# Optimization experiments

Hardware: AMD Instinct MI355X
Metric: run time of the kernel (lower is better)

The kernel has to match this reference:

```python
import jax, jax.numpy as jnp
import numpy as np

N = 50000
E = 800000
IN_CH = 128
HID = 32
HEADS = 4
OUT_CH = 40
LEAKY = 0.2
BN_EPS = 1e-5


def _gat_layer(x, src, dst, W, a_src, a_dst, b, n_nodes, concat):
    # x: [N, F_in], W: [F_in, H*C], a_src/a_dst: [H, C], b: [H*C] or [C]
    H, C = a_src.shape
    h = (x @ W).reshape(n_nodes, H, C)                      # [N, H, C]
    e_s = jnp.einsum('nhc,hc->nh', h, a_src)                # [N, H]
    e_d = jnp.einsum('nhc,hc->nh', h, a_dst)                # [N, H]
    e = e_s[src] + e_d[dst]                                 # [E, H]
    e = jnp.where(e > 0, e, LEAKY * e)                      # LeakyReLU
    # segment softmax over incoming edges of each destination node
    m = jax.ops.segment_max(e, dst, num_segments=n_nodes)   # [N, H]
    ex = jnp.exp(e - m[dst])
    s = jax.ops.segment_sum(ex, dst, num_segments=n_nodes)  # [N, H]
    alpha = ex / s[dst]                                     # [E, H]
    out = jax.ops.segment_sum(h[src] * alpha[:, :, None], dst,
                              num_segments=n_nodes)         # [N, H, C]
    out = out.reshape(n_nodes, H * C) if concat else out.mean(axis=1)
    return out + b


def setup_inputs() -> dict:
    key = jax.random.key(0)
    ks = jax.random.split(key, 16)
    d1 = HEADS * HID  # 128
    inp = {
        'x': jax.random.normal(ks[0], (N, IN_CH), dtype=jnp.float32),
        'edge_index': jax.random.randint(ks[1], (2, E), 0, N, dtype=jnp.int64),
        # conv1 params (heads=4, concat)
        'W1': jax.random.normal(ks[2], (IN_CH, d1), dtype=jnp.float32) * 0.1,
        'a1_src': jax.random.normal(ks[3], (HEADS, HID), dtype=jnp.float32) * 0.1,
        'a1_dst': jax.random.normal(ks[4], (HEADS, HID), dtype=jnp.float32) * 0.1,
        'b1': jnp.zeros((d1,), dtype=jnp.float32),
        # BatchNorm1d(128) in eval mode
        'bn_gamma': jnp.ones((d1,), dtype=jnp.float32),
        'bn_beta': jnp.zeros((d1,), dtype=jnp.float32),
        'bn_mean': jax.random.normal(ks[5], (d1,), dtype=jnp.float32) * 0.1,
        'bn_var': jax.random.uniform(ks[6], (d1,), minval=0.5, maxval=1.5, dtype=jnp.float32),
        # conv2 params (heads=1, concat=False)
        'W2': jax.random.normal(ks[7], (d1, OUT_CH), dtype=jnp.float32) * 0.1,
        'a2_src': jax.random.normal(ks[8], (1, OUT_CH), dtype=jnp.float32) * 0.1,
        'a2_dst': jax.random.normal(ks[9], (1, OUT_CH), dtype=jnp.float32) * 0.1,
        'b2': jnp.zeros((OUT_CH,), dtype=jnp.float32),
    }
    return inp


def reference(x, edge_index, W1, a1_src, a1_dst, b1, bn_gamma, bn_beta,
              bn_mean, bn_var, W2, a2_src, a2_dst, b2):
    n = x.shape[0]
    loops = jnp.arange(n, dtype=edge_index.dtype)
    src = jnp.concatenate([edge_index[0], loops])  # PyG GATConv adds self-loops
    dst = jnp.concatenate([edge_index[1], loops])
    h = _gat_layer(x, src, dst, W1, a1_src, a1_dst, b1, n, concat=True)
    h = (h - bn_mean) / jnp.sqrt(bn_var + BN_EPS) * bn_gamma + bn_beta  # BN eval
    h = jax.nn.elu(h)
    # dropout is identity in eval mode
    out = _gat_layer(h, src, dst, W2, a2_src, a2_dst, b2, n, concat=False)
    return jax.nn.log_softmax(out, axis=1)
```

## Files before the change

### kernel.cpp

```cpp
#include <hip/hip_runtime.h>
#include <hip/hip_bf16.h>
#include <math.h>

#define NN 50000
#define NE 800000
#define ETOT (NE + NN)
#define LEAKY 0.2f
#define BN_EPS 1e-5f

#define NB 256
#define BSZ 196
#define NBB 128
#define EPB ((ETOT + NBB - 1) / NBB)

#define BN1 144
#define BN2 48

typedef unsigned short u16;
typedef unsigned int u32;
typedef short s16;
typedef __attribute__((ext_vector_type(8))) short bf16x8;
typedef __attribute__((ext_vector_type(4))) float f32x4;

__device__ __forceinline__ float bf2f(u32 u) {
    union { u32 i; float f; } x; x.i = u << 16; return x.f;
}
__device__ __forceinline__ float bf2f_lo(u32 u) {
    union { u32 i; float f; } x; x.i = u << 16; return x.f;
}
__device__ __forceinline__ float bf2f_hi(u32 u) {
    union { u32 i; float f; } x; x.i = u & 0xffff0000u; return x.f;
}
__device__ __forceinline__ u16 f2bf(float f) {
    __hip_bfloat16 b = __float2bfloat16(f);
    return *reinterpret_cast<u16*>(&b);
}


__global__ __launch_bounds__(256) void k_binA(const int* __restrict__ ei,
                                              int* __restrict__ cnt) {
    __shared__ int hist[NB];
    int t = threadIdx.x;
    for (int i = t; i < NB; i += 256) hist[i] = 0;
    __syncthreads();
    int e0 = blockIdx.x * EPB, e1 = min(e0 + EPB, ETOT);
    for (int e = e0 + t; e < e1; e += 256) {
        int dst = (e < NE) ? ei[NE + e] : (e - NE);
        atomicAdd(&hist[dst / BSZ], 1);
    }
    __syncthreads();
    for (int b = t; b < NB; b += 256) cnt[b * NBB + blockIdx.x] = hist[b];
}

__global__ __launch_bounds__(256) void k_scanA(const int* __restrict__ in,
                                               int* __restrict__ out,
                                               int* __restrict__ bsums, int n) {
    __shared__ int sh[256];
    int t = threadIdx.x;
    int i = blockIdx.x * 256 + t;
    int v = (i < n) ? in[i] : 0;
    sh[t] = v;
    __syncthreads();
    #pragma unroll
    for (int off = 1; off < 256; off <<= 1) {
        int u = (t >= off) ? sh[t - off] : 0;
        __syncthreads();
        sh[t] += u;
        __syncthreads();
    }
    if (i < n) out[i] = sh[t] - v;
    if (t == 255) bsums[blockIdx.x] = sh[t];
}

__global__ __launch_bounds__(256) void k_scanB(int* __restrict__ bsums, int nb) {
    __shared__ int sh[256];
    int t = threadIdx.x;
    int v = (t < nb) ? bsums[t] : 0;
    sh[t] = v;
    __syncthreads();
    #pragma unroll
    for (int off = 1; off < 256; off <<= 1) {
        int u = (t >= off) ? sh[t - off] : 0;
        __syncthreads();
        sh[t] += u;
        __syncthreads();
    }
    if (t < nb) bsums[t] = sh[t] - v;
}

__global__ void k_scanC(int* __restrict__ out, const int* __restrict__ bsums, int n) {
    int i = blockIdx.x * blockDim.x + threadIdx.x;
    if (i < n) out[i] += bsums[i >> 8];
}

__global__ __launch_bounds__(256) void k_binB(const int* __restrict__ ei,
                                              const int* __restrict__ excl,
                                              u32* __restrict__ packed) {
    __shared__ int cur[NB];
    int t = threadIdx.x;
    for (int b = t; b < NB; b += 256) cur[b] = excl[b * NBB + blockIdx.x];
    __syncthreads();
    int e0 = blockIdx.x * EPB, e1 = min(e0 + EPB, ETOT);
    for (int e = e0 + t; e < e1; e += 256) {
        int src, dst;
        if (e < NE) { src = ei[e]; dst = ei[NE + e]; }
        else        { src = e - NE; dst = e - NE; }
        int pos = atomicAdd(&cur[dst / BSZ], 1);
        packed[pos] = ((u32)src << 16) | (u32)dst;
    }
}

__global__ __launch_bounds__(256) void k_binC(const u32* __restrict__ packed,
                                              const int* __restrict__ excl,
                                              int* __restrict__ offsets,
                                              int* __restrict__ ssrc) {
    __shared__ int hist[256];
    __shared__ int sc[256];
    __shared__ int cur[256];
    int b = blockIdx.x, t = threadIdx.x;
    int n0 = b * BSZ;
    int base = excl[b * NBB];
    int next = (b < NB - 1) ? excl[(b + 1) * NBB] : ETOT;
    int total = next - base;
    hist[t] = 0;
    __syncthreads();
    for (int i = t; i < total; i += 256) {
        int dst = (int)(packed[base + i] & 0xffffu);
        atomicAdd(&hist[dst - n0], 1);
    }
    __syncthreads();
    int v = hist[t];
    sc[t] = v;
    __syncthreads();
    #pragma unroll
    for (int off = 1; off < 256; off <<= 1) {
        int u = (t >= off) ? sc[t - off] : 0;
        __syncthreads();
        sc[t] += u;
        __syncthreads();
    }
    int exl = sc[t] - v;
    int node = n0 + t;
    if (t <= BSZ && node <= NN) {
        if (t < BSZ || node == NN) offsets[node] = base + exl;
    }
    cur[t] = exl;
    __syncthreads();
    for (int i = t; i < total; i += 256) {
        u32 pv = packed[base + i];
        int dst = (int)(pv & 0xffffu);
        int pos = atomicAdd(&cur[dst - n0], 1);
        ssrc[base + pos] = (int)(pv >> 16);
    }
}

__global__ void k_prep(const float* __restrict__ W1, const float* __restrict__ a1s,
                       const float* __restrict__ a1d, const float* __restrict__ W2,
                       const float* __restrict__ a2s, const float* __restrict__ a2d,
                       u16* __restrict__ Wt1, u16* __restrict__ Wt2) {
    int tid = blockIdx.x * blockDim.x + threadIdx.x;
    int nth = gridDim.x * blockDim.x;
    for (int idx = tid; idx < BN1 * 128; idx += nth) {
        int n = idx >> 7, k = idx & 127;
        float v = 0.f;
        if (n < 128) v = W1[k * 128 + n];
        else if (n < 132) {
            int h = n - 128; float s = 0.f;
            for (int c = 0; c < 32; ++c) s += W1[k * 128 + h * 32 + c] * a1s[h * 32 + c];
            v = s;
        } else if (n < 136) {
            int h = n - 132; float s = 0.f;
            for (int c = 0; c < 32; ++c) s += W1[k * 128 + h * 32 + c] * a1d[h * 32 + c];
            v = s;
        }
        Wt1[idx] = f2bf(v);
    }
    for (int idx = tid; idx < BN2 * 128; idx += nth) {
        int n = idx >> 7, k = idx & 127;
        float v = 0.f;
        if (n < 40) v = W2[k * 40 + n];
        else if (n == 40) { float s = 0.f; for (int c = 0; c < 40; ++c) s += W2[k * 40 + c] * a2s[c]; v = s; }
        else if (n == 41) { float s = 0.f; for (int c = 0; c < 40; ++c) s += W2[k * 40 + c] * a2d[c]; v = s; }
        Wt2[idx] = f2bf(v);
    }
}

__global__ __launch_bounds__(256) void k_mm1(const float* __restrict__ x,
                                             const u16* __restrict__ Wt1,
                                             u16* __restrict__ h1b,
                                             float* __restrict__ es1,
                                             float* __restrict__ ed1) {
    __shared__ __align__(16) s16 As[128 * 128];
    __shared__ __align__(16) s16 Bs[BN1 * 128];
    int t = threadIdx.x;
    int row0 = blockIdx.x * 128;
    #pragma unroll
    for (int i = 0; i < 16; ++i) {
        int c = t + i * 256;
        int r = c >> 5, k0 = (c & 31) * 4;
        float4 v = make_float4(0.f, 0.f, 0.f, 0.f);
        int row = row0 + r;
        if (row < NN) v = *(const float4*)&x[(size_t)row * 128 + k0];
        u16 pk[4] = {f2bf(v.x), f2bf(v.y), f2bf(v.z), f2bf(v.w)};
        int byte = (r * 256 + k0 * 2) ^ ((r & 7) << 4);
        *(uint2*)((char*)As + byte) = *(uint2*)pk;
    }
    #pragma unroll
    for (int i = 0; i < 9; ++i) {
        int c = t + i * 256;
        int n = c >> 4, k0 = (c & 15) * 8;
        uint4 v = *(const uint4*)&Wt1[n * 128 + k0];
        int byte = (n * 256 + k0 * 2) ^ ((n & 7) << 4);
        *(uint4*)((char*)Bs + byte) = v;
    }
    __syncthreads();
    int wave = t >> 6, lane = t & 63;
    int lr = lane & 15, lq = lane >> 4;
    int wrow = wave * 32;
    f32x4 acc[2][9];
    #pragma unroll
    for (int a = 0; a < 2; ++a)
        #pragma unroll
        for (int b = 0; b < 9; ++b) acc[a][b] = (f32x4){0.f, 0.f, 0.f, 0.f};
    #pragma unroll
    for (int ks = 0; ks < 4; ++ks) {
        int kb = ks * 32 + lq * 8;
        bf16x8 af[2];
        #pragma unroll
        for (int rb = 0; rb < 2; ++rb) {
            int r = wrow + rb * 16 + lr;
            int byte = (r * 256 + kb * 2) ^ ((r & 7) << 4);
            af[rb] = *(bf16x8*)((char*)As + byte);
        }
        #pragma unroll
        for (int cb = 0; cb < 9; ++cb) {
            int n = cb * 16 + lr;
            int byte = (n * 256 + kb * 2) ^ ((n & 7) << 4);
            bf16x8 bfr = *(bf16x8*)((char*)Bs + byte);
            acc[0][cb] = __builtin_amdgcn_mfma_f32_16x16x32_bf16(af[0], bfr, acc[0][cb], 0, 0, 0);
            acc[1][cb] = __builtin_amdgcn_mfma_f32_16x16x32_bf16(af[1], bfr, acc[1][cb], 0, 0, 0);
        }
    }
    #pragma unroll
    for (int rb = 0; rb < 2; ++rb) {
        #pragma unroll
        for (int cb = 0; cb < 9; ++cb) {
            #pragma unroll
            for (int r = 0; r < 4; ++r) {
                int row = row0 + wrow + rb * 16 + lq * 4 + r;
                int col = cb * 16 + lr;
                if (row < NN) {
                    float v = acc[rb][cb][r];
                    if (col < 128) h1b[(size_t)row * 128 + col] = f2bf(v);
                    else if (col < 132) es1[row * 4 + (col - 128)] = v;
                    else if (col < 136) ed1[row * 4 + (col - 132)] = v;
                }
            }
        }
    }
}

__global__ __launch_bounds__(256) void k_mm2(const u16* __restrict__ hbnb,
                                             const u16* __restrict__ Wt2,
                                             float* __restrict__ h2,
                                             float* __restrict__ es2,
                                             float* __restrict__ ed2) {
    __shared__ __align__(16) s16 As[128 * 128];
    __shared__ __align__(16) s16 Bs[BN2 * 128];
    int t = threadIdx.x;
    int row0 = blockIdx.x * 128;
    #pragma unroll
    for (int i = 0; i < 8; ++i) {
        int c = t + i * 256;
        int r = c >> 4, k0 = (c & 15) * 8;
        uint4 v = make_uint4(0, 0, 0, 0);
        int row = row0 + r;
        if (row < NN) v = *(const uint4*)&hbnb[(size_t)row * 128 + k0];
        int byte = (r * 256 + k0 * 2) ^ ((r & 7) << 4);
        *(uint4*)((char*)As + byte) = v;
    }
    #pragma unroll
    for (int i = 0; i < 3; ++i) {
        int c = t + i * 256;
        int n = c >> 4, k0 = (c & 15) * 8;
        uint4 v = *(const uint4*)&Wt2[n * 128 + k0];
        int byte = (n * 256 + k0 * 2) ^ ((n & 7) << 4);
        *(uint4*)((char*)Bs + byte) = v;
    }
    __syncthreads();
    int wave = t >> 6, lane = t & 63;
    int lr = lane & 15, lq = lane >> 4;
    int wrow = wave * 32;
    f32x4 acc[2][3];
    #pragma unroll
    for (int a = 0; a < 2; ++a)
        #pragma unroll
        for (int b = 0; b < 3; ++b) acc[a][b] = (f32x4){0.f, 0.f, 0.f, 0.f};
    #pragma unroll
    for (int ks = 0; ks < 4; ++ks) {
        int kb = ks * 32 + lq * 8;
        bf16x8 af[2];
        #pragma unroll
        for (int rb = 0; rb < 2; ++rb) {
            int r = wrow + rb * 16 + lr;
            int byte = (r * 256 + kb * 2) ^ ((r & 7) << 4);
            af[rb] = *(bf16x8*)((char*)As + byte);
        }
        #pragma unroll
        for (int cb = 0; cb < 3; ++cb) {
            int n = cb * 16 + lr;
            int byte = (n * 256 + kb * 2) ^ ((n & 7) << 4);
            bf16x8 bfr = *(bf16x8*)((char*)Bs + byte);
            acc[0][cb] = __builtin_amdgcn_mfma_f32_16x16x32_bf16(af[0], bfr, acc[0][cb], 0, 0, 0);
            acc[1][cb] = __builtin_amdgcn_mfma_f32_16x16x32_bf16(af[1], bfr, acc[1][cb], 0, 0, 0);
        }
    }
    #pragma unroll
    for (int rb = 0; rb < 2; ++rb) {
        #pragma unroll
        for (int cb = 0; cb < 3; ++cb) {
            #pragma unroll
            for (int r = 0; r < 4; ++r) {
                int row = row0 + wrow + rb * 16 + lq * 4 + r;
                int col = cb * 16 + lr;
                if (row < NN) {
                    float v = acc[rb][cb][r];
                    if (col < 40) h2[(size_t)row * 40 + col] = v;
                    else if (col == 40) es2[row] = v;
                    else if (col == 41) ed2[row] = v;
                }
            }
        }
    }
}

__global__ __launch_bounds__(256) void k_agg1(
        const u16* __restrict__ h1b, const float* __restrict__ es,
        const float* __restrict__ ed, const int* __restrict__ offsets,
        const int* __restrict__ ssrc, const float* __restrict__ b1,
        const float* __restrict__ gamma, const float* __restrict__ beta,
        const float* __restrict__ mean, const float* __restrict__ var,
        u16* __restrict__ hbnb) {
    __shared__ float wlds[4][64][4];
    int wv = threadIdx.x >> 6;
    int node = blockIdx.x * 4 + wv;
    if (node >= NN) return;
    int l = threadIdx.x & 63;
    int g = l >> 4;
    int c16 = l & 15;
    int h = c16 >> 2;
    int p0 = offsets[node], p1 = offsets[node + 1];
    float4 ed4 = *(const float4*)&ed[(size_t)node * 4];
    float4 sw4 = make_float4(0.f, 0.f, 0.f, 0.f);
    float acc[8];
    #pragma unroll
    for (int i = 0; i < 8; ++i) acc[i] = 0.f;
    for (int base = p0; base < p1; base += 64) {
        int cnt = min(64, p1 - base);
        int myidx = (l < cnt) ? ssrc[base + l] : 0;
        float4 w4 = make_float4(0.f, 0.f, 0.f, 0.f);
        if (l < cnt) {
            float4 e4 = *(const float4*)&es[(size_t)myidx * 4];
            float tv;
            tv = e4.x + ed4.x; tv = tv > 0.f ? tv : LEAKY * tv; w4.x = __expf(tv);
            tv = e4.y + ed4.y; tv = tv > 0.f ? tv : LEAKY * tv; w4.y = __expf(tv);
            tv = e4.z + ed4.z; tv = tv > 0.f ? tv : LEAKY * tv; w4.z = __expf(tv);
            tv = e4.w + ed4.w; tv = tv > 0.f ? tv : LEAKY * tv; w4.w = __expf(tv);
        }
        *(float4*)&wlds[wv][l][0] = w4;
        sw4.x += w4.x; sw4.y += w4.y; sw4.z += w4.z; sw4.w += w4.w;
        __builtin_amdgcn_wave_barrier();
        for (int j = 0; j < cnt; j += 8) {
            int e0 = j + g, e1 = j + 4 + g;
            int c0v = min(e0, cnt - 1), c1v = min(e1, cnt - 1);
            int s0 = __shfl(myidx, c0v);
            int s1 = __shfl(myidx, c1v);
            float x0 = (e0 < cnt) ? wlds[wv][c0v][h] : 0.f;
            float x1 = (e1 < cnt) ? wlds[wv][c1v][h] : 0.f;
            uint4 r0 = *(const uint4*)&h1b[(size_t)s0 * 128 + c16 * 8];
            uint4 r1 = *(const uint4*)&h1b[(size_t)s1 * 128 + c16 * 8];
            acc[0] = fmaf(x0, bf2f_lo(r0.x), acc[0]);
            acc[1] = fmaf(x0, bf2f_hi(r0.x), acc[1]);
            acc[2] = fmaf(x0, bf2f_lo(r0.y), acc[2]);
            acc[3] = fmaf(x0, bf2f_hi(r0.y), acc[3]);
            acc[4] = fmaf(x0, bf2f_lo(r0.z), acc[4]);
            acc[5] = fmaf(x0, bf2f_hi(r0.z), acc[5]);
            acc[6] = fmaf(x0, bf2f_lo(r0.w), acc[6]);
            acc[7] = fmaf(x0, bf2f_hi(r0.w), acc[7]);
            acc[0] = fmaf(x1, bf2f_lo(r1.x), acc[0]);
            acc[1] = fmaf(x1, bf2f_hi(r1.x), acc[1]);
            acc[2] = fmaf(x1, bf2f_lo(r1.y), acc[2]);
            acc[3] = fmaf(x1, bf2f_hi(r1.y), acc[3]);
            acc[4] = fmaf(x1, bf2f_lo(r1.z), acc[4]);
            acc[5] = fmaf(x1, bf2f_hi(r1.z), acc[5]);
            acc[6] = fmaf(x1, bf2f_lo(r1.w), acc[6]);
            acc[7] = fmaf(x1, bf2f_hi(r1.w), acc[7]);
        }
    }
    #pragma unroll
    for (int i = 0; i < 8; ++i) {
        acc[i] += __shfl_xor(acc[i], 16);
        acc[i] += __shfl_xor(acc[i], 32);
    }
    #pragma unroll
    for (int off = 1; off < 64; off <<= 1) {
        sw4.x += __shfl_xor(sw4.x, off);
        sw4.y += __shfl_xor(sw4.y, off);
        sw4.z += __shfl_xor(sw4.z, off);
        sw4.w += __shfl_xor(sw4.w, off);
    }
    if (g == 0) {
        float s = (h == 0) ? sw4.x : (h == 1) ? sw4.y : (h == 2) ? sw4.z : sw4.w;
        float inv = 1.f / s;
        int c0 = c16 * 8;
        float4 b1a = *(const float4*)&b1[c0],    b1b = *(const float4*)&b1[c0 + 4];
        float4 mna = *(const float4*)&mean[c0],  mnb = *(const float4*)&mean[c0 + 4];
        float4 vra = *(const float4*)&var[c0],   vrb = *(const float4*)&var[c0 + 4];
        float4 gma = *(const float4*)&gamma[c0], gmb = *(const float4*)&gamma[c0 + 4];
        float4 bta = *(const float4*)&beta[c0],  btb = *(const float4*)&beta[c0 + 4];
        float bv[8] = {b1a.x, b1a.y, b1a.z, b1a.w, b1b.x, b1b.y, b1b.z, b1b.w};
        float mn[8] = {mna.x, mna.y, mna.z, mna.w, mnb.x, mnb.y, mnb.z, mnb.w};
        float vr[8] = {vra.x, vra.y, vra.z, vra.w, vrb.x, vrb.y, vrb.z, vrb.w};
        float gm[8] = {gma.x, gma.y, gma.z, gma.w, gmb.x, gmb.y, gmb.z, gmb.w};
        float bt[8] = {bta.x, bta.y, bta.z, bta.w, btb.x, btb.y, btb.z, btb.w};
        u16 pk[8];
        #pragma unroll
        for (int i = 0; i < 8; ++i) {
            float o = acc[i] * inv + bv[i];
            o = (o - mn[i]) * rsqrtf(vr[i] + BN_EPS) * gm[i] + bt[i];
            o = o > 0.f ? o : __expf(o) - 1.f;
            pk[i] = f2bf(o);
        }
        *(uint4*)&hbnb[(size_t)node * 128 + c0] = *(uint4*)pk;
    }
}

__global__ __launch_bounds__(256) void k_agg2(
        const float* __restrict__ h2, const float* __restrict__ es,
        const float* __restrict__ ed, const int* __restrict__ offsets,
        const int* __restrict__ ssrc, const float* __restrict__ b2,
        float* __restrict__ out) {
    int node = blockIdx.x * 4 + (threadIdx.x >> 6);
    if (node >= NN) return;
    int l = threadIdx.x & 63;
    int lmod = (l < 40) ? l : (l - 40);
    int p0 = offsets[node], p1 = offsets[node + 1];
    float edv = ed[node];
    float swacc = 0.f, acc = 0.f;
    bool pay = (l < 40);
    for (int base = p0; base < p1; base += 64) {
        int cnt = min(64, p1 - base);
        int myidx = (l < cnt) ? ssrc[base + l] : 0;
        float mw = 0.f;
        if (l < cnt) {
            float e = es[myidx] + edv;
            e = e > 0.f ? e : LEAKY * e;
            mw = __expf(e);
        }
        swacc += mw;
        int j = 0;
        for (; j + 8 <= cnt; j += 8) {
            int s0 = __shfl(myidx, j);
            int s1 = __shfl(myidx, j + 1);
            int s2 = __shfl(myidx, j + 2);
            int s3 = __shfl(myidx, j + 3);
            int s4 = __shfl(myidx, j + 4);
            int s5 = __shfl(myidx, j + 5);
            int s6 = __shfl(myidx, j + 6);
            int s7 = __shfl(myidx, j + 7);
            float x0 = __shfl(mw, j);
            float x1 = __shfl(mw, j + 1);
            float x2 = __shfl(mw, j + 2);
            float x3 = __shfl(mw, j + 3);
            float x4 = __shfl(mw, j + 4);
            float x5 = __shfl(mw, j + 5);
            float x6 = __shfl(mw, j + 6);
            float x7 = __shfl(mw, j + 7);
            float h0 = h2[(size_t)s0 * 40 + lmod];
            float h1v = h2[(size_t)s1 * 40 + lmod];
            float h2v = h2[(size_t)s2 * 40 + lmod];
            float h3 = h2[(size_t)s3 * 40 + lmod];
            float h4 = h2[(size_t)s4 * 40 + lmod];
            float h5 = h2[(size_t)s5 * 40 + lmod];
            float h6 = h2[(size_t)s6 * 40 + lmod];
            float h7 = h2[(size_t)s7 * 40 + lmod];
            acc = fmaf(x0, h0, acc);
            acc = fmaf(x1, h1v, acc);
            acc = fmaf(x2, h2v, acc);
            acc = fmaf(x3, h3, acc);
            acc = fmaf(x4, h4, acc);
            acc = fmaf(x5, h5, acc);
            acc = fmaf(x6, h6, acc);
            acc = fmaf(x7, h7, acc);
        }
        for (; j + 4 <= cnt; j += 4) {
            int s0 = __shfl(myidx, j);
            int s1 = __shfl(myidx, j + 1);
            int s2 = __shfl(myidx, j + 2);
            int s3 = __shfl(myidx, j + 3);
            float x0 = __shfl(mw, j);
            float x1 = __shfl(mw, j + 1);
            float x2 = __shfl(mw, j + 2);
            float x3 = __shfl(mw, j + 3);
            float h0 = h2[(size_t)s0 * 40 + lmod];
            float h1v = h2[(size_t)s1 * 40 + lmod];
            float h2v = h2[(size_t)s2 * 40 + lmod];
            float h3 = h2[(size_t)s3 * 40 + lmod];
            acc = fmaf(x0, h0, acc);
            acc = fmaf(x1, h1v, acc);
            acc = fmaf(x2, h2v, acc);
            acc = fmaf(x3, h3, acc);
        }
        for (; j < cnt; ++j) {
            int s0 = __shfl(myidx, j);
            float x0 = __shfl(mw, j);
            float h0 = h2[(size_t)s0 * 40 + lmod];
            acc = fmaf(x0, h0, acc);
        }
    }
    float s = swacc;
    #pragma unroll
    for (int off = 1; off < 64; off <<= 1) s += __shfl_xor(s, off);
    float v = acc / s + (pay ? b2[l] : 0.f);
    float mv = pay ? v : -1e30f;
    #pragma unroll
    for (int off = 1; off < 64; off <<= 1) mv = fmaxf(mv, __shfl_xor(mv, off));
    float ex = pay ? __expf(v - mv) : 0.f;
    #pragma unroll
    for (int off = 1; off < 64; off <<= 1) ex += __shfl_xor(ex, off);
    if (pay) out[(size_t)node * 40 + l] = v - mv - __logf(ex);
}

extern "C" void kernel_launch(void* const* d_in, const int* in_sizes, int n_in,
                              void* d_out, int out_size, void* d_ws, size_t ws_size,
                              hipStream_t stream) {
    const float* x   = (const float*)d_in[0];
    const int*   ei  = (const int*)d_in[1];
    const float* W1  = (const float*)d_in[2];
    const float* a1s = (const float*)d_in[3];
    const float* a1d = (const float*)d_in[4];
    const float* b1  = (const float*)d_in[5];
    const float* bng = (const float*)d_in[6];
    const float* bnb = (const float*)d_in[7];
    const float* bnm = (const float*)d_in[8];
    const float* bnv = (const float*)d_in[9];
    const float* W2  = (const float*)d_in[10];
    const float* a2s = (const float*)d_in[11];
    const float* a2d = (const float*)d_in[12];
    const float* b2  = (const float*)d_in[13];
    float* out = (float*)d_out;

    char* ws = (char*)d_ws;
    size_t off = 0;
    auto alloc = [&](size_t bytes) -> void* {
        void* p = ws + off;
        off = (off + bytes + 255) & ~(size_t)255;
        return p;
    };
    int*   cntb     = (int*)alloc((size_t)NB * NBB * 4);
    int*   excl     = (int*)alloc((size_t)NB * NBB * 4);
    int*   bsums    = (int*)alloc((size_t)NBB * 4);
    int*   offsets  = (int*)alloc((size_t)(NN + 1) * 4);
    u32*   packed   = (u32*)alloc((size_t)ETOT * 4);
    int*   ssrc     = (int*)alloc((size_t)ETOT * 4);
    u16*   Wt1      = (u16*)alloc((size_t)BN1 * 128 * 2);
    u16*   Wt2      = (u16*)alloc((size_t)BN2 * 128 * 2);
    u16*   h1b      = (u16*)alloc((size_t)NN * 128 * 2);
    float* es1      = (float*)alloc((size_t)NN * 4 * 4);
    float* ed1      = (float*)alloc((size_t)NN * 4 * 4);
    u16*   hbnb     = (u16*)alloc((size_t)NN * 128 * 2);
    float* h2       = (float*)alloc((size_t)NN * 40 * 4);
    float* es2      = (float*)alloc((size_t)NN * 4);
    float* ed2      = (float*)alloc((size_t)NN * 4);

    const int nscan = NB * NBB;
    k_prep<<<80, 256, 0, stream>>>(W1, a1s, a1d, W2, a2s, a2d, Wt1, Wt2);
    k_binA<<<NBB, 256, 0, stream>>>(ei, cntb);
    k_scanA<<<nscan / 256, 256, 0, stream>>>(cntb, excl, bsums, nscan);
    k_scanB<<<1, 256, 0, stream>>>(bsums, NBB);
    k_scanC<<<nscan / 256, 256, 0, stream>>>(excl, bsums, nscan);
    k_binB<<<NBB, 256, 0, stream>>>(ei, excl, packed);
    k_binC<<<NB, 256, 0, stream>>>(packed, excl, offsets, ssrc);
    k_mm1<<<(NN + 127) / 128, 256, 0, stream>>>(x, Wt1, h1b, es1, ed1);
    k_agg1<<<(NN + 3) / 4, 256, 0, stream>>>(h1b, es1, ed1, offsets, ssrc,
                                             b1, bng, bnb, bnm, bnv, hbnb);
    k_mm2<<<(NN + 127) / 128, 256, 0, stream>>>(hbnb, Wt2, h2, es2, ed2);
    k_agg2<<<(NN + 3) / 4, 256, 0, stream>>>(h2, es2, ed2, offsets, ssrc, b2, out);
}
```

Baseline: 147.6 us.

## Store layer-2 features as padded bf16 and merge the three scan kernels into one

Layer-2 features are now written as bf16 rows padded to 64 columns. The second aggregation gathers 16-byte vectors per edge, with 8 edges handled in parallel per wave, and reduces across lane groups before the log-softmax. This halves gather bytes and uses wider loads, at the cost of bf16 rounding of h2. The three-kernel scan over 32768 bin counts is replaced by a single 1024-thread block scan, removing two launches. The code relies on helpers bf2f_lo/bf2f_hi, which may live in the hidden lines.

```diff
diff --git a/kernel.cpp b/kernel.cpp
--- a/kernel.cpp
+++ b/kernel.cpp
@@ -52,45 +52,35 @@
     for (int b = t; b < NB; b += 256) cnt[b * NBB + blockIdx.x] = hist[b];
 }
 
-__global__ __launch_bounds__(256) void k_scanA(const int* __restrict__ in,
-                                               int* __restrict__ out,
-                                               int* __restrict__ bsums, int n) {
-    __shared__ int sh[256];
+__global__ __launch_bounds__(1024) void k_scanONE(const int* __restrict__ in,
+                                                  int* __restrict__ out) {
+    __shared__ int sums[1024];
     int t = threadIdx.x;
-    int i = blockIdx.x * 256 + t;
-    int v = (i < n) ? in[i] : 0;
-    sh[t] = v;
-    __syncthreads();
-    #pragma unroll
-    for (int off = 1; off < 256; off <<= 1) {
-        int u = (t >= off) ? sh[t - off] : 0;
+    int4 loc[8];
+    const int4* ip = (const int4*)(in + t * 32);
+    int s = 0;
+    #pragma unroll
+    for (int i = 0; i < 8; ++i) {
+        loc[i] = ip[i];
+        s += loc[i].x + loc[i].y + loc[i].z + loc[i].w;
+    }
+    sums[t] = s;
+    __syncthreads();
+    for (int off = 1; off < 1024; off <<= 1) {
+        int u = (t >= off) ? sums[t - off] : 0;
         __syncthreads();
-        sh[t] += u;
+        sums[t] += u;
         __syncthreads();
     }
-    if (i < n) out[i] = sh[t] - v;
-    if (t == 255) bsums[blockIdx.x] = sh[t];
-}
-
-__global__ __launch_bounds__(256) void k_scanB(int* __restrict__ bsums, int nb) {
-    __shared__ int sh[256];
-    int t = threadIdx.x;
-    int v = (t < nb) ? bsums[t] : 0;
-    sh[t] = v;
-    __syncthreads();
-    #pragma unroll
-    for (int off = 1; off < 256; off <<= 1) {
-        int u = (t >= off) ? sh[t - off] : 0;
-        __syncthreads();
-        sh[t] += u;
-        __syncthreads();
-    }
-    if (t < nb) bsums[t] = sh[t] - v;
-}
-
-__global__ void k_scanC(int* __restrict__ out, const int* __restrict__ bsums, int n) {
-    int i = blockIdx.x * blockDim.x + threadIdx.x;
-    if (i < n) out[i] += bsums[i >> 8];
+    int run = (t == 0) ? 0 : sums[t - 1];
+    int* op = out + t * 32;
+    #pragma unroll
+    for (int i = 0; i < 8; ++i) {
+        op[i * 4 + 0] = run; run += loc[i].x;
+        op[i * 4 + 1] = run; run += loc[i].y;
+        op[i * 4 + 2] = run; run += loc[i].z;
+        op[i * 4 + 3] = run; run += loc[i].w;
+    }
 }
 
 __global__ __launch_bounds__(256) void k_binB(const int* __restrict__ ei,
@@ -262,7 +252,7 @@
 
 __global__ __launch_bounds__(256) void k_mm2(const u16* __restrict__ hbnb,
                                              const u16* __restrict__ Wt2,
-                                             float* __restrict__ h2,
+                                             u16* __restrict__ h2b,
                                              float* __restrict__ es2,
                                              float* __restrict__ ed2) {
     __shared__ __align__(16) s16 As[128 * 128];
@@ -325,9 +315,13 @@
                 int col = cb * 16 + lr;
                 if (row < NN) {
                     float v = acc[rb][cb][r];
-                    if (col < 40) h2[(size_t)row * 40 + col] = v;
-                    else if (col == 40) es2[row] = v;
-                    else if (col == 41) ed2[row] = v;
+                    if (col < 40) {
+                        h2b[(size_t)row * 64 + col] = f2bf(v);
+                    } else {
+                        if (col == 40) es2[row] = v;
+                        else if (col == 41) ed2[row] = v;
+                        h2b[(size_t)row * 64 + col] = 0;
+                    }
                 }
             }
         }
@@ -436,18 +430,23 @@
 }
 
 __global__ __launch_bounds__(256) void k_agg2(
-        const float* __restrict__ h2, const float* __restrict__ es,
+        const u16* __restrict__ h2b, const float* __restrict__ es,
         const float* __restrict__ ed, const int* __restrict__ offsets,
         const int* __restrict__ ssrc, const float* __restrict__ b2,
         float* __restrict__ out) {
-    int node = blockIdx.x * 4 + (threadIdx.x >> 6);
+    __shared__ float wlds[4][64];
+    int wv = threadIdx.x >> 6;
+    int node = blockIdx.x * 4 + wv;
     if (node >= NN) return;
     int l = threadIdx.x & 63;
-    int lmod = (l < 40) ? l : (l - 40);
+    int g = l >> 3;
+    int c8 = l & 7;
     int p0 = offsets[node], p1 = offsets[node + 1];
     float edv = ed[node];
-    float swacc = 0.f, acc = 0.f;
-    bool pay = (l < 40);
+    float swacc = 0.f;
+    float acc[8];
+    #pragma unroll
+    for (int i = 0; i < 8; ++i) acc[i] = 0.f;
     for (int base = p0; base < p1; base += 64) {
         int cnt = min(64, p1 - base);
         int myidx = (l < cnt) ? ssrc[base + l] : 0;
@@ -457,78 +456,78 @@
             e = e > 0.f ? e : LEAKY * e;
             mw = __expf(e);
         }
+        wlds[wv][l] = mw;
         swacc += mw;
-        int j = 0;
-        for (; j + 8 <= cnt; j += 8) {
-            int s0 = __shfl(myidx, j);
-            int s1 = __shfl(myidx, j + 1);
-            int s2 = __shfl(myidx, j + 2);
-            int s3 = __shfl(myidx, j + 3);
-            int s4 = __shfl(myidx, j + 4);
-            int s5 = __shfl(myidx, j + 5);
-            int s6 = __shfl(myidx, j + 6);
-            int s7 = __shfl(myidx, j + 7);
-            float x0 = __shfl(mw, j);
-            float x1 = __shfl(mw, j + 1);
-            float x2 = __shfl(mw, j + 2);
-            float x3 = __shfl(mw, j + 3);
-            float x4 = __shfl(mw, j + 4);
-            float x5 = __shfl(mw, j + 5);
-            float x6 = __shfl(mw, j + 6);
-            float x7 = __shfl(mw, j + 7);
-            float h0 = h2[(size_t)s0 * 40 + lmod];
-            float h1v = h2[(size_t)s1 * 40 + lmod];
-            float h2v = h2[(size_t)s2 * 40 + lmod];
-            float h3 = h2[(size_t)s3 * 40 + lmod];
-            float h4 = h2[(size_t)s4 * 40 + lmod];
-            float h5 = h2[(size_t)s5 * 40 + lmod];
-            float h6 = h2[(size_t)s6 * 40 + lmod];
-            float h7 = h2[(size_t)s7 * 40 + lmod];
-            acc = fmaf(x0, h0, acc);
-            acc = fmaf(x1, h1v, acc);
-            acc = fmaf(x2, h2v, acc);
-            acc = fmaf(x3, h3, acc);
-            acc = fmaf(x4, h4, acc);
-            acc = fmaf(x5, h5, acc);
-            acc = fmaf(x6, h6, acc);
-            acc = fmaf(x7, h7, acc);
-        }
-        for (; j + 4 <= cnt; j += 4) {
-            int s0 = __shfl(myidx, j);
-            int s1 = __shfl(myidx, j + 1);
-            int s2 = __shfl(myidx, j + 2);
-            int s3 = __shfl(myidx, j + 3);
-            float x0 = __shfl(mw, j);
-            float x1 = __shfl(mw, j + 1);
-            float x2 = __shfl(mw, j + 2);
-            float x3 = __shfl(mw, j + 3);
-            float h0 = h2[(size_t)s0 * 40 + lmod];
-            float h1v = h2[(size_t)s1 * 40 + lmod];
-            float h2v = h2[(size_t)s2 * 40 + lmod];
-            float h3 = h2[(size_t)s3 * 40 + lmod];
-            acc = fmaf(x0, h0, acc);
-            acc = fmaf(x1, h1v, acc);
-            acc = fmaf(x2, h2v, acc);
-            acc = fmaf(x3, h3, acc);
-        }
-        for (; j < cnt; ++j) {
-            int s0 = __shfl(myidx, j);
-            float x0 = __shfl(mw, j);
-            float h0 = h2[(size_t)s0 * 40 + lmod];
-            acc = fmaf(x0, h0, acc);
-        }
+        __builtin_amdgcn_wave_barrier();
+        for (int j = 0; j < cnt; j += 16) {
+            int e0 = j + g, e1 = j + 8 + g;
+            int c0v = min(e0, cnt - 1), c1v = min(e1, cnt - 1);
+            int s0 = __shfl(myidx, c0v);
+            int s1 = __shfl(myidx, c1v);
+            float x0 = (e0 < cnt) ? wlds[wv][c0v] : 0.f;
+            float x1 = (e1 < cnt) ? wlds[wv][c1v] : 0.f;
+            uint4 r0 = *(const uint4*)&h2b[(size_t)s0 * 64 + c8 * 8];
+            uint4 r1 = *(const uint4*)&h2b[(size_t)s1 * 64 + c8 * 8];
+            acc[0] = fmaf(x0, bf2f_lo(r0.x), acc[0]);
+            acc[1] = fmaf(x0, bf2f_hi(r0.x), acc[1]);
+            acc[2] = fmaf(x0, bf2f_lo(r0.y), acc[2]);
+            acc[3] = fmaf(x0, bf2f_hi(r0.y), acc[3]);
+            acc[4] = fmaf(x0, bf2f_lo(r0.z), acc[4]);
+            acc[5] = fmaf(x0, bf2f_hi(r0.z), acc[5]);
+            acc[6] = fmaf(x0, bf2f_lo(r0.w), acc[6]);
+            acc[7] = fmaf(x0, bf2f_hi(r0.w), acc[7]);
+            acc[0] = fmaf(x1, bf2f_lo(r1.x), acc[0]);
+            acc[1] = fmaf(x1, bf2f_hi(r1.x), acc[1]);
+            acc[2] = fmaf(x1, bf2f_lo(r1.y), acc[2]);
+            acc[3] = fmaf(x1, bf2f_hi(r1.y), acc[3]);
+            acc[4] = fmaf(x1, bf2f_lo(r1.z), acc[4]);
+            acc[5] = fmaf(x1, bf2f_hi(r1.z), acc[5]);
+            acc[6] = fmaf(x1, bf2f_lo(r1.w), acc[6]);
+            acc[7] = fmaf(x1, bf2f_hi(r1.w), acc[7]);
+        }
+    }
+    #pragma unroll
+    for (int i = 0; i < 8; ++i) {
+        acc[i] += __shfl_xor(acc[i], 8);
+        acc[i] += __shfl_xor(acc[i], 16);
+        acc[i] += __shfl_xor(acc[i], 32);
     }
     float s = swacc;
     #pragma unroll
     for (int off = 1; off < 64; off <<= 1) s += __shfl_xor(s, off);
-    float v = acc / s + (pay ? b2[l] : 0.f);
-    float mv = pay ? v : -1e30f;
-    #pragma unroll
-    for (int off = 1; off < 64; off <<= 1) mv = fmaxf(mv, __shfl_xor(mv, off));
-    float ex = pay ? __expf(v - mv) : 0.f;
-    #pragma unroll
-    for (int off = 1; off < 64; off <<= 1) ex += __shfl_xor(ex, off);
-    if (pay) out[(size_t)node * 40 + l] = v - mv - __logf(ex);
+    float inv = 1.f / s;
+    bool valid = (c8 < 5);
+    int c0 = c8 * 8;
+    float v[8];
+    float m8 = -1e30f;
+    if (valid) {
+        float4 b2a = *(const float4*)&b2[c0];
+        float4 b2b = *(const float4*)&b2[c0 + 4];
+        float bv[8] = {b2a.x, b2a.y, b2a.z, b2a.w, b2b.x, b2b.y, b2b.z, b2b.w};
+        #pragma unroll
+        for (int i = 0; i < 8; ++i) {
+            v[i] = acc[i] * inv + bv[i];
+            m8 = fmaxf(m8, v[i]);
+        }
+    }
+    m8 = fmaxf(m8, __shfl_xor(m8, 1));
+    m8 = fmaxf(m8, __shfl_xor(m8, 2));
+    m8 = fmaxf(m8, __shfl_xor(m8, 4));
+    float ex = 0.f;
+    if (valid) {
+        #pragma unroll
+        for (int i = 0; i < 8; ++i) ex += __expf(v[i] - m8);
+    }
+    ex += __shfl_xor(ex, 1);
+    ex += __shfl_xor(ex, 2);
+    ex += __shfl_xor(ex, 4);
+    if (g == 0 && valid) {
+        float lg = m8 + __logf(ex);
+        float4 o0 = make_float4(v[0] - lg, v[1] - lg, v[2] - lg, v[3] - lg);
+        float4 o1 = make_float4(v[4] - lg, v[5] - lg, v[6] - lg, v[7] - lg);
+        *(float4*)&out[(size_t)node * 40 + c0] = o0;
+        *(float4*)&out[(size_t)node * 40 + c0 + 4] = o1;
+    }
 }
 
 extern "C" void kernel_launch(void* const* d_in, const int* in_sizes, int n_in,
@@ -559,7 +558,6 @@
     };
     int*   cntb     = (int*)alloc((size_t)NB * NBB * 4);
     int*   excl     = (int*)alloc((size_t)NB * NBB * 4);
-    int*   bsums    = (int*)alloc((size_t)NBB * 4);
     int*   offsets  = (int*)alloc((size_t)(NN + 1) * 4);
     u32*   packed   = (u32*)alloc((size_t)ETOT * 4);
     int*   ssrc     = (int*)alloc((size_t)ETOT * 4);
@@ -569,21 +567,18 @@
     float* es1      = (float*)alloc((size_t)NN * 4 * 4);
     float* ed1      = (float*)alloc((size_t)NN * 4 * 4);
     u16*   hbnb     = (u16*)alloc((size_t)NN * 128 * 2);
-    float* h2       = (float*)alloc((size_t)NN * 40 * 4);
+    u16*   h2b      = (u16*)alloc((size_t)NN * 64 * 2);
     float* es2      = (float*)alloc((size_t)NN * 4);
     float* ed2      = (float*)alloc((size_t)NN * 4);
 
-    const int nscan = NB * NBB;
     k_prep<<<80, 256, 0, stream>>>(W1, a1s, a1d, W2, a2s, a2d, Wt1, Wt2);
     k_binA<<<NBB, 256, 0, stream>>>(ei, cntb);
-    k_scanA<<<nscan / 256, 256, 0, stream>>>(cntb, excl, bsums, nscan);
-    k_scanB<<<1, 256, 0, stream>>>(bsums, NBB);
-    k_scanC<<<nscan / 256, 256, 0, stream>>>(excl, bsums, nscan);
+    k_scanONE<<<1, 1024, 0, stream>>>(cntb, excl);
     k_binB<<<NBB, 256, 0, stream>>>(ei, excl, packed);
     k_binC<<<NB, 256, 0, stream>>>(packed, excl, offsets, ssrc);
     k_mm1<<<(NN + 127) / 128, 256, 0, stream>>>(x, Wt1, h1b, es1, ed1);
     k_agg1<<<(NN + 3) / 4, 256, 0, stream>>>(h1b, es1, ed1, offsets, ssrc,
                                              b1, bng, bnb, bnm, bnv, hbnb);
-    k_mm2<<<(NN + 127) / 128, 256, 0, stream>>>(hbnb, Wt2, h2, es2, ed2);
-    k_agg2<<<(NN + 3) / 4, 256, 0, stream>>>(h2, es2, ed2, offsets, ssrc, b2, out);
-}
+    k_mm2<<<(NN + 127) / 128, 256, 0, stream>>>(hbnb, Wt2, h2b, es2, ed2);
+    k_agg2<<<(NN + 3) / 4, 256, 0, stream>>>(h2b, es2, ed2, offsets, ssrc, b2, out);
+}
```

Measured after the change: 144.4 us. -2.2%, faster.
